# Optimization experiments

Measured on AMD Instinct MI355X. Metric: run time of the kernel, lower is better.

The kernel has to match this reference:

```python
import jax, jax.numpy as jnp
import numpy as np

RADIUS = 0.2
NSAMPLE = 32
USE_XYZ = True

B, N, S, C = 8, 8192, 2048, 64


def setup_inputs() -> dict:
    key = jax.random.key(0)
    k1, k2, k3 = jax.random.split(key, 3)
    xyz = jax.random.uniform(k1, (B, N, 3), dtype=jnp.float32)
    new_xyz = jax.random.uniform(k2, (B, S, 3), dtype=jnp.float32)
    features = jax.random.normal(k3, (B, N, C), dtype=jnp.float32)
    return {"xyz": xyz, "new_xyz": new_xyz, "features": features}


def _ball_query(new_xyz, xyz, radius, nsample):
    # new_xyz: (B,S,3), xyz: (B,N,3) -> idx (B,S,nsample) int32
    n = xyz.shape[1]
    d2 = jnp.sum((new_xyz[:, :, None, :] - xyz[:, None, :, :]) ** 2, axis=-1)  # (B,S,N)
    mask = d2 < radius * radius
    # keys: index j if inside ball else N (sentinel); smallest nsample keys = first
    # nsample in-ball indices in ascending j order (matches CUDA ball_query order).
    keys = jnp.where(mask, jnp.arange(n, dtype=jnp.int32), jnp.int32(n))
    neg_vals, _ = jax.lax.top_k(-keys, nsample)  # top_k of -keys -> smallest keys
    idx = -neg_vals  # (B,S,nsample), ascending
    first = idx[..., 0:1]
    idx = jnp.where(idx == n, first, idx)   # pad empty slots with first hit
    idx = jnp.where(idx == n, 0, idx)       # balls with zero hits -> index 0
    return idx


def _group(points, idx):
    # points: (B,N,D), idx: (B,S,K) -> (B,S,K,D)
    return jax.vmap(lambda p, i: p[i])(points, idx)


def reference(xyz, new_xyz, features):
    idx = _ball_query(new_xyz, xyz, RADIUS, NSAMPLE)
    grouped_xyz = _group(xyz, idx) - new_xyz[:, :, None, :]  # (B,S,K,3)
    grouped_feat = _group(features, idx)                      # (B,S,K,C)
    if USE_XYZ:
        new_features = jnp.concatenate([grouped_xyz, grouped_feat], axis=-1)
    else:
        new_features = grouped_feat
    return jnp.transpose(new_features, (0, 3, 1, 2))  # (B, C+3, S, K)
```

## Files before the change

kernel.cpp:

```cpp
#include <hip/hip_runtime.h>

#define BB 8
#define NN 8192
#define SS 2048
#define CC 64
#define NS 32
#define COUT 67

__global__ __launch_bounds__(256) void qg_kernel(
    const float* __restrict__ xyz,
    const float* __restrict__ new_xyz,
    const float* __restrict__ feat,
    float* __restrict__ out)
{
#pragma clang fp contract(off)
    __shared__ int idx_sh[4][NS];
    const int wave = threadIdx.x >> 6;
    const int lane = threadIdx.x & 63;
    const int qid  = blockIdx.x * 4 + wave;
    const int b = qid >> 11;
    const int s = qid & 2047;

    const float R2 = 0.04f;

    const float* ctr = new_xyz + ((size_t)b * SS + s) * 3;
    const float cx = ctr[0], cy = ctr[1], cz = ctr[2];

    const float* xb = xyz + (size_t)b * NN * 3;

    int total = 0;
    int firstIdx = 0;
    for (int j0 = 0; j0 < NN && total < NS; j0 += 64) {
        const int j = j0 + lane;
        const float* p = xb + (size_t)j * 3;
        const float dx = p[0] - cx;
        const float dy = p[1] - cy;
        const float dz = p[2] - cz;
        float d2 = dx * dx;
        d2 = d2 + dy * dy;
        d2 = d2 + dz * dz;
        const bool hit = d2 < R2;
        const unsigned long long mask = __ballot(hit);
        if (total == 0 && mask != 0ull)
            firstIdx = j0 + __builtin_ctzll(mask);
        if (hit) {
            const int pos = total + __popcll(mask & ((1ull << lane) - 1ull));
            if (pos < NS) idx_sh[wave][pos] = j;
        }
        total += __popcll(mask);
    }
    if (total < NS) {
        const int fill = (total > 0) ? firstIdx : 0;
        if (lane >= total && lane < NS) idx_sh[wave][lane] = fill;
    }

    const int k = lane & 31;
    const int h = lane >> 5;
    const int ik = idx_sh[wave][k];

    const size_t plane = (size_t)SS * NS;

    if (h == 0) {
        const float* p = xb + (size_t)ik * 3;
        const size_t ob = (((size_t)b * COUT + 0) * SS + s) * NS + k;
        out[ob]             = p[0] - cx;
        out[ob + plane]     = p[1] - cy;
        out[ob + 2 * plane] = p[2] - cz;
    }

    const float* frow = feat + ((size_t)b * NN + ik) * CC;
    const size_t obase = (((size_t)b * COUT + 3) * SS + s) * NS + k;
    for (int cf = 0; cf < CC; cf += 8) {
        const int c0 = cf + 4 * h;
        const float4 f = *(const float4*)(frow + c0);
        const size_t o = obase + (size_t)c0 * plane;
        out[o]             = f.x;
        out[o + plane]     = f.y;
        out[o + 2 * plane] = f.z;
        out[o + 3 * plane] = f.w;
    }
}

extern "C" void kernel_launch(void* const* d_in, const int* in_sizes, int n_in,
                              void* d_out, int out_size, void* d_ws, size_t ws_size,
                              hipStream_t stream) {
    const float* xyz     = (const float*)d_in[0];
    const float* new_xyz = (const float*)d_in[1];
    const float* feat    = (const float*)d_in[2];
    float* out = (float*)d_out;
    qg_kernel<<<dim3((BB * SS) / 4), dim3(256), 0, stream>>>(xyz, new_xyz, feat, out);
}
```

Before: 217.1 us.

## Split ball query and gather into separate kernels, unroll scan by four

Splits the fused kernel in two. A scan kernel writes neighbor indices to workspace, and a gather kernel reads them back to write the grouped output. The scan loop now processes four 64-point chunks per iteration so several loads are in flight before the ballots. This is meant to separate the latency-bound scan from the bandwidth-bound gather and raise memory-level parallelism. In exchange it adds a second launch, a workspace round trip, and up to 192 wasted distance computations past the early exit.

```diff
diff --git a/kernel.cpp b/kernel.cpp
--- a/kernel.cpp
+++ b/kernel.cpp
@@ -7,14 +7,12 @@
 #define NS 32
 #define COUT 67
 
-__global__ __launch_bounds__(256) void qg_kernel(
+__global__ __launch_bounds__(256) void scan_kernel(
     const float* __restrict__ xyz,
     const float* __restrict__ new_xyz,
-    const float* __restrict__ feat,
-    float* __restrict__ out)
+    int* __restrict__ idx_ws)
 {
 #pragma clang fp contract(off)
-    __shared__ int idx_sh[4][NS];
     const int wave = threadIdx.x >> 6;
     const int lane = threadIdx.x & 63;
     const int qid  = blockIdx.x * 4 + wave;
@@ -25,38 +23,68 @@
 
     const float* ctr = new_xyz + ((size_t)b * SS + s) * 3;
     const float cx = ctr[0], cy = ctr[1], cz = ctr[2];
-
     const float* xb = xyz + (size_t)b * NN * 3;
 
+    int* myidx = idx_ws + (size_t)qid * NS;
+    const unsigned long long lt = (1ull << lane) - 1ull;
+
     int total = 0;
-    int firstIdx = 0;
-    for (int j0 = 0; j0 < NN && total < NS; j0 += 64) {
-        const int j = j0 + lane;
-        const float* p = xb + (size_t)j * 3;
-        const float dx = p[0] - cx;
-        const float dy = p[1] - cy;
-        const float dz = p[2] - cz;
-        float d2 = dx * dx;
-        d2 = d2 + dy * dy;
-        d2 = d2 + dz * dz;
-        const bool hit = d2 < R2;
-        const unsigned long long mask = __ballot(hit);
-        if (total == 0 && mask != 0ull)
-            firstIdx = j0 + __builtin_ctzll(mask);
-        if (hit) {
-            const int pos = total + __popcll(mask & ((1ull << lane) - 1ull));
-            if (pos < NS) idx_sh[wave][pos] = j;
+    int firstIdx = -1;
+    for (int j0 = 0; j0 < NN && total < NS; j0 += 256) {
+        float d2v[4];
+#pragma unroll
+        for (int u = 0; u < 4; ++u) {
+            const int j = j0 + u * 64 + lane;
+            const float* p = xb + (size_t)j * 3;
+            const float dx = p[0] - cx;
+            const float dy = p[1] - cy;
+            const float dz = p[2] - cz;
+            float d2 = dx * dx;
+            d2 = d2 + dy * dy;
+            d2 = d2 + dz * dz;
+            d2v[u] = d2;
         }
-        total += __popcll(mask);
+#pragma unroll
+        for (int u = 0; u < 4; ++u) {
+            const bool hit = d2v[u] < R2;
+            const unsigned long long mask = __ballot(hit);
+            if (firstIdx < 0 && mask != 0ull)
+                firstIdx = j0 + u * 64 + __builtin_ctzll(mask);
+            if (hit) {
+                const int pos = total + __popcll(mask & lt);
+                if (pos < NS) myidx[pos] = j0 + u * 64 + lane;
+            }
+            total += __popcll(mask);
+        }
     }
     if (total < NS) {
         const int fill = (total > 0) ? firstIdx : 0;
-        if (lane >= total && lane < NS) idx_sh[wave][lane] = fill;
+        if (lane >= total && lane < NS) myidx[lane] = fill;
     }
+}
+
+__global__ __launch_bounds__(256) void gather_kernel(
+    const float* __restrict__ xyz,
+    const float* __restrict__ new_xyz,
+    const float* __restrict__ feat,
+    const int* __restrict__ idx_ws,
+    float* __restrict__ out)
+{
+#pragma clang fp contract(off)
+    const int wave = threadIdx.x >> 6;
+    const int lane = threadIdx.x & 63;
+    const int qid  = blockIdx.x * 4 + wave;
+    const int b = qid >> 11;
+    const int s = qid & 2047;
 
     const int k = lane & 31;
     const int h = lane >> 5;
-    const int ik = idx_sh[wave][k];
+
+    const int ik = idx_ws[(size_t)qid * NS + k];
+
+    const float* ctr = new_xyz + ((size_t)b * SS + s) * 3;
+    const float cx = ctr[0], cy = ctr[1], cz = ctr[2];
+    const float* xb = xyz + (size_t)b * NN * 3;
 
     const size_t plane = (size_t)SS * NS;
 
@@ -88,5 +116,8 @@
     const float* new_xyz = (const float*)d_in[1];
     const float* feat    = (const float*)d_in[2];
     float* out = (float*)d_out;
-    qg_kernel<<<dim3((BB * SS) / 4), dim3(256), 0, stream>>>(xyz, new_xyz, feat, out);
+    int* idx_ws = (int*)d_ws;
+
+    scan_kernel<<<dim3((BB * SS) / 4), dim3(256), 0, stream>>>(xyz, new_xyz, idx_ws);
+    gather_kernel<<<dim3((BB * SS) / 4), dim3(256), 0, stream>>>(xyz, new_xyz, feat, idx_ws, out);
 }
```

Result: faster. 196.0 us (-9.7%).
